# Performance work log

Hardware: AMD Instinct MI355X
Metric: run time of the kernel (lower is better)

Reference implementation:

```python
import jax, jax.numpy as jnp
import numpy as np

T, D, H, HD = 4096, 1536, 12, 128  # tokens, hidden, heads, head_dim
NEG = -1e9


def rotate_half(x):
    x1, x2 = jnp.split(x, 2, axis=-1)
    return jnp.concatenate((-x2, x1), axis=-1)


def setup_inputs() -> dict:
    key = jax.random.key(0)
    k1, k2, k3, k4 = jax.random.split(key, 4)
    hidden_states = jax.random.normal(k1, (T, D), dtype=jnp.float32)
    cu_seqlens = (jnp.arange(5, dtype=jnp.int32) * (T // 4))  # [0,1024,2048,3072,4096]
    # rotary angles: positions within each segment times inverse frequencies
    pos = jnp.arange(T, dtype=jnp.float32) % (T // 4)
    inv_freq = 1.0 / (10000.0 ** (jnp.arange(0, HD // 2, dtype=jnp.float32) / (HD // 2)))
    rotary_pos_emb = pos[:, None] * inv_freq[None, :]  # (T, HD//2)
    w_qkv = jax.random.normal(k2, (3 * D, D), dtype=jnp.float32) * (D ** -0.5)
    w_proj = jax.random.normal(k3, (D, D), dtype=jnp.float32) * (D ** -0.5)
    return {"hidden_states": hidden_states, "cu_seqlens": cu_seqlens,
            "rotary_pos_emb": rotary_pos_emb, "w_qkv": w_qkv, "w_proj": w_proj}


def reference(hidden_states, cu_seqlens, rotary_pos_emb, w_qkv, w_proj):
    seq_len = hidden_states.shape[0]
    scaling = HD ** -0.5
    # fused QKV projection: (T, 3D) -> (3, T, H, HD)
    qkv = (hidden_states @ w_qkv.T).reshape(seq_len, 3, H, HD).transpose(1, 0, 2, 3)
    q, k, v = qkv[0], qkv[1], qkv[2]
    # RoPE (vision style): emb = cat(rpe, rpe) along last dim
    emb = jnp.concatenate((rotary_pos_emb, rotary_pos_emb), axis=-1)  # (T, HD)
    cos = jnp.cos(emb)[:, None, :]  # (T, 1, HD) broadcast over heads
    sin = jnp.sin(emb)[:, None, :]
    q = q * cos + rotate_half(q) * sin
    k = k * cos + rotate_half(k) * sin
    # block-diagonal mask from cu_seqlens (varlen packing)
    seg_id = jnp.searchsorted(cu_seqlens[1:], jnp.arange(seq_len), side="right")
    block_mask = seg_id[:, None] == seg_id[None, :]  # (T, T) bool
    # attention per head: (H, T, HD)
    qh = q.transpose(1, 0, 2)
    kh = k.transpose(1, 0, 2)
    vh = v.transpose(1, 0, 2)
    scores = jnp.einsum("htd,hsd->hts", qh, kh) * scaling
    scores = jnp.where(block_mask[None, :, :], scores, NEG)
    attn = jax.nn.softmax(scores, axis=-1)
    out = jnp.einsum("hts,hsd->htd", attn, vh)  # (H, T, HD)
    out = out.transpose(1, 0, 2).reshape(seq_len, D)
    return out @ w_proj.T


if __name__ == "__main__":
    o = reference(**setup_inputs())
    print(o.shape, o.dtype)
```

## Files before the change

### kernel.cpp

```cpp
#include <hip/hip_runtime.h>
#include <stdint.h>

#define TT 4096
#define DD 1536
#define NH 12
#define HD_ 128

typedef __bf16 bf16x8 __attribute__((ext_vector_type(8)));
typedef float  f32x4  __attribute__((ext_vector_type(4)));
typedef float  f32x16 __attribute__((ext_vector_type(16)));

__device__ __forceinline__ unsigned short f2b(float f) {
  union { float f; uint32_t u; } x; x.f = f;
  uint32_t r = x.u + 0x7fffu + ((x.u >> 16) & 1u);
  return (unsigned short)(r >> 16);
}
__device__ __forceinline__ float b2f(unsigned short b) {
  union { uint32_t u; float f; } x; x.u = ((uint32_t)b) << 16;
  return x.f;
}

__device__ __forceinline__ f32x16 mfma32(bf16x8 a, bf16x8 b, f32x16 c) {
  return __builtin_amdgcn_mfma_f32_32x32x16_bf16(a, b, c, 0, 0, 0);
}

__device__ __forceinline__ void async16(const void* g, void* l) {
  __builtin_amdgcn_global_load_lds((const __attribute__((address_space(1))) uint32_t*)g,
                                   (__attribute__((address_space(3))) uint32_t*)l,
                                   16, 0, 0);
}

__global__ void cast_bf16_kernel(const float* __restrict__ in,
                                 unsigned short* __restrict__ out, int n) {
  int i = (blockIdx.x * blockDim.x + threadIdx.x) * 4;
  if (i + 3 < n) {
    float4 v = *reinterpret_cast<const float4*>(in + i);
    ushort4 o;
    o.x = f2b(v.x); o.y = f2b(v.y); o.z = f2b(v.z); o.w = f2b(v.w);
    *reinterpret_cast<ushort4*>(out + i) = o;
  }
}

__global__ __launch_bounds__(256) void gemm_qkv_kernel(
    const unsigned short* __restrict__ A, const unsigned short* __restrict__ B,
    unsigned short* __restrict__ Qp, unsigned short* __restrict__ Kp,
    unsigned short* __restrict__ Vp) {
  __shared__ unsigned short lA[128 * 32];
  __shared__ unsigned short lB[128 * 32];
  const int tid = threadIdx.x;
  const int lane = tid & 63;
  const int wave = tid >> 6;
  const int wm = wave >> 1, wn = wave & 1;
  const int lr = lane & 15, lh = lane >> 4;
  const int m0 = blockIdx.x * 128, n0 = blockIdx.y * 128;
  const unsigned short* Ag = A + (size_t)(m0 + (tid >> 2)) * DD + (tid & 3) * 8;
  const unsigned short* Bg = B + (size_t)(n0 + (tid >> 2)) * DD + (tid & 3) * 8;
  f32x4 acc[4][4] = {};
  for (int k0 = 0; k0 < DD; k0 += 32) {
    async16(Ag + k0, &lA[tid * 8]);
    async16(Ag + k0 + (size_t)64 * DD, &lA[2048 + tid * 8]);
    async16(Bg + k0, &lB[tid * 8]);
    async16(Bg + k0 + (size_t)64 * DD, &lB[2048 + tid * 8]);
    __syncthreads();
    bf16x8 af[4], bfr[4];
#pragma unroll
    for (int i = 0; i < 4; i++) {
      af[i]  = *reinterpret_cast<const bf16x8*>(&lA[(wm * 64 + i * 16 + lr) * 32 + lh * 8]);
      bfr[i] = *reinterpret_cast<const bf16x8*>(&lB[(wn * 64 + i * 16 + lr) * 32 + lh * 8]);
    }
#pragma unroll
    for (int i = 0; i < 4; i++)
#pragma unroll
      for (int j = 0; j < 4; j++)
        acc[i][j] = __builtin_amdgcn_mfma_f32_16x16x32_bf16(af[i], bfr[j], acc[i][j], 0, 0, 0);
    __syncthreads();
  }
#pragma unroll
  for (int i = 0; i < 4; i++) {
#pragma unroll
    for (int j = 0; j < 4; j++) {
      int cn = n0 + wn * 64 + j * 16 + lr;
      int s = cn / DD;
      int rem = cn - s * DD;
      int hh = rem >> 7;
      int dd = rem & 127;
      unsigned short* dst = (s == 0) ? Qp : ((s == 1) ? Kp : Vp);
#pragma unroll
      for (int r = 0; r < 4; r++) {
        int t = m0 + wm * 64 + i * 16 + lh * 4 + r;
        dst[((size_t)hh * TT + t) * HD_ + dd] = f2b(acc[i][j][r]);
      }
    }
  }
}

__global__ __launch_bounds__(256) void transpose_v_kernel(
    const unsigned short* __restrict__ V, unsigned short* __restrict__ Vt) {
  __shared__ unsigned short tile[32][33];
  const int h = blockIdx.z;
  const int t0 = blockIdx.y * 32;
  const int d0 = blockIdx.x * 32;
  const int tx = threadIdx.x & 31, ty = threadIdx.x >> 5;
#pragma unroll
  for (int k = 0; k < 4; k++)
    tile[ty + 8 * k][tx] = V[((size_t)h * TT + t0 + ty + 8 * k) * HD_ + d0 + tx];
  __syncthreads();
#pragma unroll
  for (int k = 0; k < 4; k++)
    Vt[((size_t)h * HD_ + d0 + ty + 8 * k) * TT + t0 + tx] = tile[tx][ty + 8 * k];
}

__global__ __launch_bounds__(64) void rope_kernel(unsigned short* __restrict__ Qp,
                                                  unsigned short* __restrict__ Kp,
                                                  const float* __restrict__ rpe) {
  const int t = blockIdx.x;
  const int d2 = threadIdx.x;
  float e = rpe[t * 64 + d2];
  float sn, cs;
  sincosf(e, &sn, &cs);
  const float scale = 0.08838834764831845f * 1.4426950408889634f;
#pragma unroll
  for (int h = 0; h < NH; h++) {
    size_t base = ((size_t)h * TT + t) * HD_ + d2;
    float qlo = b2f(Qp[base]), qhi = b2f(Qp[base + 64]);
    Qp[base]      = f2b((qlo * cs - qhi * sn) * scale);
    Qp[base + 64] = f2b((qhi * cs + qlo * sn) * scale);
    float klo = b2f(Kp[base]), khi = b2f(Kp[base + 64]);
    Kp[base]      = f2b(klo * cs - khi * sn);
    Kp[base + 64] = f2b(khi * cs + klo * sn);
  }
}

__global__ __launch_bounds__(512) void attn_kernel(
    const unsigned short* __restrict__ Qp, const unsigned short* __restrict__ Kp,
    const unsigned short* __restrict__ Vt, const int* __restrict__ cu,
    unsigned short* __restrict__ AO) {
  __shared__ unsigned short lds[32768];
  const int bid = blockIdx.x;
  const int tid = threadIdx.x;
  const int wave = tid >> 6;
  const int lane = tid & 63;
  const int lq = lane & 31;
  const int hi = lane >> 5;
  const int swz = lq & 7;

  const int xcd  = bid & 7;
  const int idx  = bid >> 3;
  const int pair = xcd * 6 + (idx >> 2);
  const int qblk = idx & 3;
  const int h    = pair >> 2;
  const int seg  = pair & 3;
  const int kstart = cu[seg], kend = cu[seg + 1];
  const int q0 = kstart + (qblk * 8 + wave) * 32;

  const unsigned short* Kh = Kp + (size_t)h * TT * HD_;
  const unsigned short* Vh = Vt + (size_t)h * HD_ * TT;

  const int krow0 = tid >> 4, kc0 = tid & 15;
  const int vrow0 = tid >> 3, vc0 = tid & 7;

#define STAGE_TILE(BUF, KT)                                                    \
  {                                                                            \
    unsigned short* Lk = &lds[(BUF) * 16384];                                  \
    unsigned short* Lv = Lk + 8192;                                            \
    _Pragma("unroll")                                                          \
    for (int r = 0; r < 2; r++) {                                              \
      int row = krow0 + r * 32;                                                \
      int c = kc0 ^ (row & 7);                                                 \
      async16(Kh + (size_t)((KT) + row) * HD_ + c * 8, Lk + tid * 8 + r * 4096); \
    }                                                                          \
    _Pragma("unroll")                                                          \
    for (int r = 0; r < 2; r++) {                                              \
      int row = vrow0 + r * 64;                                                \
      int c = vc0 ^ (row & 7);                                                 \
      async16(Vh + (size_t)row * TT + (KT) + c * 8, Lv + tid * 8 + r * 4096);  \
    }                                                                          \
  }

  const unsigned short* Qg = Qp + ((size_t)h * TT + q0 + lq) * HD_ + hi * 8;
  bf16x8 qf[8];
#pragma unroll
  for (int s = 0; s < 8; s++)
    qf[s] = *reinterpret_cast<const bf16x8*>(Qg + s * 16);

  STAGE_TILE(0, kstart);
  __syncthreads();

  f32x16 o0 = {}, o1 = {}, o2 = {}, o3 = {};
  float lsum = 0.f;
  int cur = 0;

  for (int kt = kstart; kt < kend; kt += 64) {
    const int ktn = (kt + 64 < kend) ? (kt + 64) : kt;
    STAGE_TILE(cur ^ 1, ktn);

    const unsigned short* Kl = &lds[cur * 16384];
    const unsigned short* Vl = Kl + 8192;

    f32x16 sA = {}, sB = {};
#pragma unroll
    for (int s = 0; s < 8; s++) {
      bf16x8 kf = *reinterpret_cast<const bf16x8*>(
          Kl + lq * 128 + (((s << 1) | hi) ^ swz) * 8);
      sA = mfma32(kf, qf[s], sA);
    }
#pragma unroll
    for (int s = 0; s < 8; s++) {
      bf16x8 kf = *reinterpret_cast<const bf16x8*>(
          Kl + 4096 + lq * 128 + (((s << 1) | hi) ^ swz) * 8);
      sB = mfma32(kf, qf[s], sB);
    }

    bf16x8 pfrag[4];
    float acc0 = 0.f, acc1 = 0.f;
#pragma unroll
    for (int g = 0; g < 4; g++) {
      const f32x16 S = (g & 2) ? sB : sA;
      const int b = (g & 1) * 8;
      float e0 = __builtin_amdgcn_exp2f(S[b + 0]);
      float e1 = __builtin_amdgcn_exp2f(S[b + 1]);
      float e2 = __builtin_amdgcn_exp2f(S[b + 2]);
      float e3 = __builtin_amdgcn_exp2f(S[b + 3]);
      float e4 = __builtin_amdgcn_exp2f(S[b + 4]);
      float e5 = __builtin_amdgcn_exp2f(S[b + 5]);
      float e6 = __builtin_amdgcn_exp2f(S[b + 6]);
      float e7 = __builtin_amdgcn_exp2f(S[b + 7]);
      acc0 += (e0 + e1) + (e2 + e3);
      acc1 += (e4 + e5) + (e6 + e7);
      union PW { uint32_t u; __bf16 e[2]; } p0, p1, p2, p3;
      p0.e[0] = (__bf16)e0; p0.e[1] = (__bf16)e1;
      p1.e[0] = (__bf16)e2; p1.e[1] = (__bf16)e3;
      p2.e[0] = (__bf16)e4; p2.e[1] = (__bf16)e5;
      p3.e[0] = (__bf16)e6; p3.e[1] = (__bf16)e7;
      uint32_t W2 = (uint32_t)__shfl_xor((int)(hi ? p0.u : p2.u), 32);
      uint32_t W3 = (uint32_t)__shfl_xor((int)(hi ? p1.u : p3.u), 32);
      union F { uint32_t w[4]; bf16x8 v; } f;
      f.w[0] = hi ? W2 : p0.u;
      f.w[1] = hi ? W3 : p1.u;
      f.w[2] = hi ? p2.u : W2;
      f.w[3] = hi ? p3.u : W3;
      pfrag[g] = f.v;
    }
    float tsum = acc0 + acc1;
    lsum += tsum + __shfl_xor(tsum, 32);

#pragma unroll
    for (int g = 0; g < 4; g++) {
      const int co = (((g << 1) | hi) ^ swz) * 8;
      bf16x8 v0 = *reinterpret_cast<const bf16x8*>(Vl + (lq)       * 64 + co);
      bf16x8 v1 = *reinterpret_cast<const bf16x8*>(Vl + (32 + lq)  * 64 + co);
      bf16x8 v2 = *reinterpret_cast<const bf16x8*>(Vl + (64 + lq)  * 64 + co);
      bf16x8 v3 = *reinterpret_cast<const bf16x8*>(Vl + (96 + lq)  * 64 + co);
      o0 = mfma32(v0, pfrag[g], o0);
      o1 = mfma32(v1, pfrag[g], o1);
      o2 = mfma32(v2, pfrag[g], o2);
      o3 = mfma32(v3, pfrag[g], o3);
    }

    __syncthreads();
    cur ^= 1;
  }
#undef STAGE_TILE

  const float inv = 1.0f / lsum;
  unsigned short* Ab = AO + (size_t)(q0 + lq) * DD + h * HD_ + 4 * hi;
#pragma unroll
  for (int dblk = 0; dblk < 4; dblk++) {
    f32x16 o = (dblk == 0) ? o0 : (dblk == 1) ? o1 : (dblk == 2) ? o2 : o3;
#pragma unroll
    for (int rq = 0; rq < 4; rq++) {
      ushort4 st;
      st.x = f2b(o[rq * 4 + 0] * inv);
      st.y = f2b(o[rq * 4 + 1] * inv);
      st.z = f2b(o[rq * 4 + 2] * inv);
      st.w = f2b(o[rq * 4 + 3] * inv);
      *reinterpret_cast<ushort4*>(Ab + dblk * 32 + rq * 8) = st;
    }
  }
}

__global__ __launch_bounds__(256) void gemm_out_kernel(
    const unsigned short* __restrict__ A, const unsigned short* __restrict__ B,
    float* __restrict__ C) {
  __shared__ unsigned short lA[128 * 32];
  __shared__ unsigned short lB[128 * 32];
  const int tid = threadIdx.x;
  const int lane = tid & 63;
  const int wave = tid >> 6;
  const int wm = wave >> 1, wn = wave & 1;
  const int lr = lane & 15, lh = lane >> 4;
  const int m0 = blockIdx.x * 128, n0 = blockIdx.y * 128;
  const unsigned short* Ag = A + (size_t)(m0 + (tid >> 2)) * DD + (tid & 3) * 8;
  const unsigned short* Bg = B + (size_t)(n0 + (tid >> 2)) * DD + (tid & 3) * 8;
  f32x4 acc[4][4] = {};
  for (int k0 = 0; k0 < DD; k0 += 32) {
    async16(Ag + k0, &lA[tid * 8]);
    async16(Ag + k0 + (size_t)64 * DD, &lA[2048 + tid * 8]);
    async16(Bg + k0, &lB[tid * 8]);
    async16(Bg + k0 + (size_t)64 * DD, &lB[2048 + tid * 8]);
    __syncthreads();
    bf16x8 af[4], bfr[4];
#pragma unroll
    for (int i = 0; i < 4; i++) {
      af[i]  = *reinterpret_cast<const bf16x8*>(&lA[(wm * 64 + i * 16 + lr) * 32 + lh * 8]);
      bfr[i] = *reinterpret_cast<const bf16x8*>(&lB[(wn * 64 + i * 16 + lr) * 32 + lh * 8]);
    }
#pragma unroll
    for (int i = 0; i < 4; i++)
#pragma unroll
      for (int j = 0; j < 4; j++)
        acc[i][j] = __builtin_amdgcn_mfma_f32_16x16x32_bf16(af[i], bfr[j], acc[i][j], 0, 0, 0);
    __syncthreads();
  }
#pragma unroll
  for (int i = 0; i < 4; i++)
#pragma unroll
    for (int j = 0; j < 4; j++) {
      int cn = n0 + wn * 64 + j * 16 + lr;
#pragma unroll
      for (int r = 0; r < 4; r++) {
        int t = m0 + wm * 64 + i * 16 + lh * 4 + r;
        C[(size_t)t * DD + cn] = acc[i][j][r];
      }
    }
}

extern "C" void kernel_launch(void* const* d_in, const int* in_sizes, int n_in,
                              void* d_out, int out_size, void* d_ws, size_t ws_size,
                              hipStream_t stream) {
  const float* hs    = (const float*)d_in[0];
  const int*   cu    = (const int*)d_in[1];
  const float* rpe   = (const float*)d_in[2];
  const float* wqkv  = (const float*)d_in[3];
  const float* wproj = (const float*)d_in[4];
  float* out = (float*)d_out;
  char* ws = (char*)d_ws;

  unsigned short* hb = (unsigned short*)(ws + 0);
  unsigned short* wq = (unsigned short*)(ws + 12582912);
  unsigned short* wp = (unsigned short*)(ws + 26738688);
  unsigned short* Qp = (unsigned short*)(ws + 31457280);
  unsigned short* Kp = (unsigned short*)(ws + 44040192);
  unsigned short* Vp = (unsigned short*)(ws + 56623104);

  cast_bf16_kernel<<<6144, 256, 0, stream>>>(hs, hb, TT * DD);
  cast_bf16_kernel<<<6912, 256, 0, stream>>>(wqkv, wq, 3 * DD * DD);
  cast_bf16_kernel<<<2304, 256, 0, stream>>>(wproj, wp, DD * DD);

  gemm_qkv_kernel<<<dim3(32, 36), 256, 0, stream>>>(hb, wq, Qp, Kp, Vp);

  transpose_v_kernel<<<dim3(4, 128, 12), 256, 0, stream>>>(Vp, wq );
  rope_kernel<<<TT, 64, 0, stream>>>(Qp, Kp, rpe);

  attn_kernel<<<192, 512, 0, stream>>>(Qp, Kp, wq , cu, hb );

  gemm_out_kernel<<<dim3(32, 12), 256, 0, stream>>>(hb , wp, out);
}
```

Measured before the change: 189.6 us.

## Fuse RoPE and V transpose into QKV GEMM epilogue with XCD-aware block mapping

The QKV GEMM epilogue now applies RoPE and the Q scaling to Q/K tiles directly, exchanging partner halves through LDS and reading precomputed cos/sin tables. It writes V already transposed as vectorized ushort4 stores. This removes the separate rope and transpose kernels and their extra global round trips. The grid is flattened and remapped so consecutive tiles land on the same XCD, and the trig tables are built in a small kernel that reuses the w_proj staging buffer before that weight is cast. The epilogue gains extra syncs and scattered per-element table reads.

```diff
diff --git a/kernel.cpp b/kernel.cpp
--- a/kernel.cpp
+++ b/kernel.cpp
@@ -41,18 +41,37 @@
   }
 }
 
+__global__ void trig_table_kernel(const float* __restrict__ rpe,
+                                  float* __restrict__ cs, float* __restrict__ sn) {
+  int i = blockIdx.x * blockDim.x + threadIdx.x;
+  float e = rpe[i];
+  float s, c;
+  sincosf(e, &s, &c);
+  cs[i] = c;
+  sn[i] = s;
+}
+
 __global__ __launch_bounds__(256) void gemm_qkv_kernel(
     const unsigned short* __restrict__ A, const unsigned short* __restrict__ B,
     unsigned short* __restrict__ Qp, unsigned short* __restrict__ Kp,
-    unsigned short* __restrict__ Vp) {
-  __shared__ unsigned short lA[128 * 32];
-  __shared__ unsigned short lB[128 * 32];
+    unsigned short* __restrict__ Vt, const float* __restrict__ csT,
+    const float* __restrict__ snT) {
+  __shared__ char smem[16384];
+  unsigned short* lA = (unsigned short*)smem;
+  unsigned short* lB = (unsigned short*)(smem + 8192);
+  float* Lf = (float*)smem;
+
   const int tid = threadIdx.x;
   const int lane = tid & 63;
   const int wave = tid >> 6;
   const int wm = wave >> 1, wn = wave & 1;
   const int lr = lane & 15, lh = lane >> 4;
-  const int m0 = blockIdx.x * 128, n0 = blockIdx.y * 128;
+
+  const int flat = blockIdx.x;
+  const int wgid = (flat & 7) * 144 + (flat >> 3);
+  const int m0 = (wgid & 31) * 128;
+  const int n0 = (wgid >> 5) * 128;
+
   const unsigned short* Ag = A + (size_t)(m0 + (tid >> 2)) * DD + (tid & 3) * 8;
   const unsigned short* Bg = B + (size_t)(n0 + (tid >> 2)) * DD + (tid & 3) * 8;
   f32x4 acc[4][4] = {};
@@ -75,59 +94,53 @@
         acc[i][j] = __builtin_amdgcn_mfma_f32_16x16x32_bf16(af[i], bfr[j], acc[i][j], 0, 0, 0);
     __syncthreads();
   }
-#pragma unroll
-  for (int i = 0; i < 4; i++) {
-#pragma unroll
-    for (int j = 0; j < 4; j++) {
-      int cn = n0 + wn * 64 + j * 16 + lr;
-      int s = cn / DD;
-      int rem = cn - s * DD;
-      int hh = rem >> 7;
-      int dd = rem & 127;
-      unsigned short* dst = (s == 0) ? Qp : ((s == 1) ? Kp : Vp);
-#pragma unroll
-      for (int r = 0; r < 4; r++) {
-        int t = m0 + wm * 64 + i * 16 + lh * 4 + r;
-        dst[((size_t)hh * TT + t) * HD_ + dd] = f2b(acc[i][j][r]);
+
+  const int s  = n0 / DD;
+  const int hh = (n0 - s * DD) >> 7;
+
+  if (s == 2) {
+#pragma unroll
+    for (int i = 0; i < 4; i++)
+#pragma unroll
+      for (int j = 0; j < 4; j++) {
+        const int dd = wn * 64 + j * 16 + lr;
+        const int t0 = m0 + wm * 64 + i * 16 + lh * 4;
+        ushort4 st;
+        st.x = f2b(acc[i][j][0]); st.y = f2b(acc[i][j][1]);
+        st.z = f2b(acc[i][j][2]); st.w = f2b(acc[i][j][3]);
+        *reinterpret_cast<ushort4*>(&Vt[((size_t)(hh * HD_ + dd)) * TT + t0]) = st;
       }
-    }
-  }
-}
-
-__global__ __launch_bounds__(256) void transpose_v_kernel(
-    const unsigned short* __restrict__ V, unsigned short* __restrict__ Vt) {
-  __shared__ unsigned short tile[32][33];
-  const int h = blockIdx.z;
-  const int t0 = blockIdx.y * 32;
-  const int d0 = blockIdx.x * 32;
-  const int tx = threadIdx.x & 31, ty = threadIdx.x >> 5;
-#pragma unroll
-  for (int k = 0; k < 4; k++)
-    tile[ty + 8 * k][tx] = V[((size_t)h * TT + t0 + ty + 8 * k) * HD_ + d0 + tx];
-  __syncthreads();
-#pragma unroll
-  for (int k = 0; k < 4; k++)
-    Vt[((size_t)h * HD_ + d0 + ty + 8 * k) * TT + t0 + tx] = tile[tx][ty + 8 * k];
-}
-
-__global__ __launch_bounds__(64) void rope_kernel(unsigned short* __restrict__ Qp,
-                                                  unsigned short* __restrict__ Kp,
-                                                  const float* __restrict__ rpe) {
-  const int t = blockIdx.x;
-  const int d2 = threadIdx.x;
-  float e = rpe[t * 64 + d2];
-  float sn, cs;
-  sincosf(e, &sn, &cs);
-  const float scale = 0.08838834764831845f * 1.4426950408889634f;
-#pragma unroll
-  for (int h = 0; h < NH; h++) {
-    size_t base = ((size_t)h * TT + t) * HD_ + d2;
-    float qlo = b2f(Qp[base]), qhi = b2f(Qp[base + 64]);
-    Qp[base]      = f2b((qlo * cs - qhi * sn) * scale);
-    Qp[base + 64] = f2b((qhi * cs + qlo * sn) * scale);
-    float klo = b2f(Kp[base]), khi = b2f(Kp[base + 64]);
-    Kp[base]      = f2b(klo * cs - khi * sn);
-    Kp[base + 64] = f2b(khi * cs + klo * sn);
+  } else {
+    unsigned short* dst = (s == 0) ? Qp : Kp;
+    const float scale =
+        (s == 0) ? (0.08838834764831845f * 1.4426950408889634f) : 1.0f;
+#pragma unroll
+    for (int i = 0; i < 4; i++) {
+      __syncthreads();
+#pragma unroll
+      for (int j = 0; j < 4; j++)
+#pragma unroll
+        for (int r = 0; r < 4; r++)
+          Lf[(wm * 16 + lh * 4 + r) * 128 + wn * 64 + j * 16 + lr] = acc[i][j][r];
+      __syncthreads();
+#pragma unroll
+      for (int j = 0; j < 4; j++) {
+        const int dd = wn * 64 + j * 16 + lr;
+        const int d2 = dd & 63;
+        const float sgn = (dd < 64) ? -1.f : 1.f;
+#pragma unroll
+        for (int r = 0; r < 4; r++) {
+          const int lrow = wm * 16 + lh * 4 + r;
+          const int t = m0 + wm * 64 + i * 16 + lh * 4 + r;
+          const float own = acc[i][j][r];
+          const float par = Lf[lrow * 128 + (dd ^ 64)];
+          const float c = csT[t * 64 + d2];
+          const float sn_ = snT[t * 64 + d2];
+          dst[((size_t)hh * TT + t) * HD_ + dd] =
+              f2b((own * c + sgn * par * sn_) * scale);
+        }
+      }
+    }
   }
 }
 
@@ -341,18 +354,20 @@
   unsigned short* wp = (unsigned short*)(ws + 26738688);
   unsigned short* Qp = (unsigned short*)(ws + 31457280);
   unsigned short* Kp = (unsigned short*)(ws + 44040192);
-  unsigned short* Vp = (unsigned short*)(ws + 56623104);
-
+  unsigned short* Vt = (unsigned short*)(ws + 56623104);
+
+  float* csT = (float*)wp;
+  float* snT = csT + TT * 64;
+
+  trig_table_kernel<<<1024, 256, 0, stream>>>(rpe, csT, snT);
   cast_bf16_kernel<<<6144, 256, 0, stream>>>(hs, hb, TT * DD);
   cast_bf16_kernel<<<6912, 256, 0, stream>>>(wqkv, wq, 3 * DD * DD);
+
+  gemm_qkv_kernel<<<1152, 256, 0, stream>>>(hb, wq, Qp, Kp, Vt, csT, snT);
+
   cast_bf16_kernel<<<2304, 256, 0, stream>>>(wproj, wp, DD * DD);
 
-  gemm_qkv_kernel<<<dim3(32, 36), 256, 0, stream>>>(hb, wq, Qp, Kp, Vp);
-
-  transpose_v_kernel<<<dim3(4, 128, 12), 256, 0, stream>>>(Vp, wq );
-  rope_kernel<<<TT, 64, 0, stream>>>(Qp, Kp, rpe);
-
-  attn_kernel<<<192, 512, 0, stream>>>(Qp, Kp, wq , cu, hb );
+  attn_kernel<<<192, 512, 0, stream>>>(Qp, Kp, Vt, cu, hb );
 
   gemm_out_kernel<<<dim3(32, 12), 256, 0, stream>>>(hb , wp, out);
 }
```

Result: slower. 328.8 us (+73.4%).
